# Kernel tuning notes

Hardware: AMD Instinct MI355X
Metric: run time of the kernel (lower is better)

The kernel has to match this reference:

```python
import jax, jax.numpy as jnp
import numpy as np

B, D = 8192, 64   # batch, state_dim (even -> canonical symplectic L)
H = 2 * D         # entropy MLP hidden


def setup_inputs() -> dict:
    key = jax.random.key(0)
    ks = jax.random.split(key, 6)
    sD = 1.0 / np.sqrt(D)
    sH = 1.0 / np.sqrt(H)
    z  = jax.random.normal(ks[0], (B, D), dtype=jnp.float32)
    # entropy MLP: Linear(D, 2D) -> SiLU -> Linear(2D, 1)  (torch default init ~ U(-1/sqrt(fan_in), ..))
    W1 = jax.random.uniform(ks[1], (H, D), jnp.float32, -sD, sD)
    b1 = jax.random.uniform(ks[2], (H,),   jnp.float32, -sD, sD)
    W2 = jax.random.uniform(ks[3], (1, H), jnp.float32, -sH, sH)
    b2 = jax.random.uniform(ks[4], (1,),   jnp.float32, -sH, sH)
    # friction A = Linear(D, D, bias=False)
    Wf = jax.random.uniform(ks[5], (D, D), jnp.float32, -sD, sD)
    return {"z": z, "W1": W1, "b1": b1, "W2": W2, "b2": b2, "Wf": Wf}


def _generic_forward(z, W1, b1, W2, b2, Wf):
    # grad_E: E = 0.5*||z||^2  ->  grad_E = z
    grad_E = z

    # grad_S via autodiff through the learnable entropy MLP (matches torch.autograd.grad)
    def entropy_sum(zz):
        h = jax.nn.silu(zz @ W1.T + b1)      # (B, 2D)
        return ((h @ W2.T) + b2).sum()       # scalar
    grad_S = jax.grad(entropy_sum)(z)        # (B, D)

    # Reversible term: canonical symplectic L (state_dim even). L is exactly skew,
    # so the 0.5*(L - L^T) projection is a no-op. L @ grad_E = [grad_E_p, -grad_E_q].
    n = D // 2
    reversible = jnp.concatenate([grad_E[:, n:], -grad_E[:, :n]], axis=-1)  # (B, D)

    # Friction: A = z Wf^T ; M = diag(A)^T diag(A) = diag(A^2); symmetrize (no-op),
    # then PSD projection via eigh + eigenvalue clamp (faithful to _make_psd).
    a = z @ Wf.T                                    # (B, D)
    M = (a * a)[:, :, None] * jnp.eye(D, dtype=z.dtype)  # diag_embed, (B, D, D)
    w, V = jnp.linalg.eigh(M)                       # batched small eigh
    w = jnp.clip(w, 0.0, None)
    M_psd = jnp.einsum('bij,bj,bkj->bik', V, w, V)  # V diag(w) V^T

    irreversible = jnp.einsum('bij,bj->bi', M_psd, grad_S)  # (B, D)

    lambda_rev = 1.0
    lambda_irr = 1.0
    return lambda_rev * reversible + lambda_irr * irreversible


def reference(z, W1, b1, W2, b2, Wf):
    return _generic_forward(z, W1, b1, W2, b2, Wf)
```

## Files before the change

kernel.cpp:

```cpp
#include <hip/hip_runtime.h>
#include <hip/hip_bf16.h>

typedef __bf16 bf16x8 __attribute__((ext_vector_type(8)));
typedef float  f32x4  __attribute__((ext_vector_type(4)));

#define MFMA16(a,b,c) __builtin_amdgcn_mfma_f32_16x16x32_bf16((a),(b),(c),0,0,0)

constexpr int Bn = 8192, Dd = 64, Hh = 128, MT = 32;

__device__ __forceinline__ unsigned short f2bf(float f) {
    unsigned int u = __builtin_bit_cast(unsigned int, f);
    u = (u + 0x7FFFu + ((u >> 16) & 1u)) >> 16;
    return (unsigned short)u;
}

__device__ __forceinline__ bf16x8 ld8(const unsigned short* p) {
    return *(const bf16x8*)p;
}

__global__ __launch_bounds__(256) void gnl_kernel(
    const float* __restrict__ z, const float* __restrict__ W1,
    const float* __restrict__ b1, const float* __restrict__ W2,
    const float* __restrict__ Wf, float* __restrict__ out)
{
    __shared__ unsigned short sh[29184];
    __shared__ float b1f[128];
    __shared__ float w2f[128];
    unsigned short* W1b = sh;
    unsigned short* Wfb = sh + 9216;
    unsigned short* Zb  = sh + 13824;
    unsigned short* W1T = sh + 16128;
    unsigned short* Gb  = sh + 24832;

    const int tid  = threadIdx.x;
    const int row0 = blockIdx.x * MT;

    {
        const float4* gv = (const float4*)W1;
        for (int i = tid; i < (Hh * Dd) / 4; i += 256) {
            float4 v = gv[i];
            int e = i << 2, j = e >> 6, d = e & 63;
            unsigned short c0 = f2bf(v.x), c1 = f2bf(v.y), c2 = f2bf(v.z), c3 = f2bf(v.w);
            *(ushort4*)(W1b + j * 72 + d) = make_ushort4(c0, c1, c2, c3);
            W1T[(d + 0) * 136 + j] = c0;
            W1T[(d + 1) * 136 + j] = c1;
            W1T[(d + 2) * 136 + j] = c2;
            W1T[(d + 3) * 136 + j] = c3;
        }
        gv = (const float4*)Wf;
        for (int i = tid; i < (Dd * Dd) / 4; i += 256) {
            float4 v = gv[i];
            int e = i << 2, j = e >> 6, d = e & 63;
            *(ushort4*)(Wfb + j * 72 + d) =
                make_ushort4(f2bf(v.x), f2bf(v.y), f2bf(v.z), f2bf(v.w));
        }
        gv = (const float4*)(z + (size_t)row0 * Dd);
        for (int i = tid; i < (MT * Dd) / 4; i += 256) {
            float4 v = gv[i];
            int e = i << 2, r = e >> 6, d = e & 63;
            *(ushort4*)(Zb + r * 72 + d) =
                make_ushort4(f2bf(v.x), f2bf(v.y), f2bf(v.z), f2bf(v.w));
        }
        if (tid < 128) { b1f[tid] = b1[tid]; w2f[tid] = W2[tid]; }
    }
    __syncthreads();

    const int lane = tid & 63, w = tid >> 6;
    const int l15 = lane & 15, q = lane >> 4;
    const int mt = w & 1;

    const int zoff = (mt * 16 + l15) * 72 + q * 8;
    bf16x8 za0 = ld8(Zb + zoff);
    bf16x8 za1 = ld8(Zb + zoff + 32);

    {
        const int ntb = (w >> 1) * 4;
        for (int nt = 0; nt < 4; ++nt) {
            const int jc = (ntb + nt) * 16 + l15;
            const unsigned short* wp = W1b + jc * 72 + q * 8;
            f32x4 acc = {0.f, 0.f, 0.f, 0.f};
            acc = MFMA16(za0, ld8(wp), acc);
            acc = MFMA16(za1, ld8(wp + 32), acc);
            const float bj = b1f[jc], w2j = w2f[jc];
            #pragma unroll
            for (int r = 0; r < 4; ++r) {
                float u = acc[r] + bj;
                float s = 1.f / (1.f + __expf(-u));
                float g = w2j * (s * (1.f + u * (1.f - s)));
                Gb[(mt * 16 + q * 4 + r) * 136 + jc] = f2bf(g);
            }
        }
    }
    __syncthreads();

    {
        const int goff = (mt * 16 + l15) * 136 + q * 8;
        bf16x8 ga0 = ld8(Gb + goff);
        bf16x8 ga1 = ld8(Gb + goff + 32);
        bf16x8 ga2 = ld8(Gb + goff + 64);
        bf16x8 ga3 = ld8(Gb + goff + 96);
        const int ntb = (w >> 1) * 2;
        for (int nt = 0; nt < 2; ++nt) {
            const int dc = (ntb + nt) * 16 + l15;
            const unsigned short* wt = W1T + dc * 136 + q * 8;
            f32x4 gs = {0.f, 0.f, 0.f, 0.f};
            gs = MFMA16(ga0, ld8(wt), gs);
            gs = MFMA16(ga1, ld8(wt + 32), gs);
            gs = MFMA16(ga2, ld8(wt + 64), gs);
            gs = MFMA16(ga3, ld8(wt + 96), gs);
            const unsigned short* wfp = Wfb + dc * 72 + q * 8;
            f32x4 av = {0.f, 0.f, 0.f, 0.f};
            av = MFMA16(za0, ld8(wfp), av);
            av = MFMA16(za1, ld8(wfp + 32), av);
            const bool  lo  = dc < 32;
            const int   src = lo ? dc + 32 : dc - 32;
            const float sgn = lo ? 1.f : -1.f;
            #pragma unroll
            for (int r = 0; r < 4; ++r) {
                const int rr = row0 + mt * 16 + q * 4 + r;
                float rev = sgn * z[(size_t)rr * Dd + src];
                float a = av[r];
                out[(size_t)rr * Dd + dc] = rev + a * a * gs[r];
            }
        }
    }
}

extern "C" void kernel_launch(void* const* d_in, const int* in_sizes, int n_in,
                              void* d_out, int out_size, void* d_ws, size_t ws_size,
                              hipStream_t stream)
{
    const float* z  = (const float*)d_in[0];
    const float* W1 = (const float*)d_in[1];
    const float* b1 = (const float*)d_in[2];
    const float* W2 = (const float*)d_in[3];
    const float* Wf = (const float*)d_in[5];
    float* out = (float*)d_out;
    gnl_kernel<<<Bn / MT, 256, 0, stream>>>(z, W1, b1, W2, Wf, out);
}
```

Baseline: 68.96 us.

## Precompute bf16 weight image once and DMA it into LDS per block

A separate prep kernel converts W1, W1^T, Wf, b1 and W2 once into a padded bf16 image in workspace. The main kernel then copies that image straight into LDS with global_load_lds instead of having every block convert and transpose the weights itself. The row tile is halved to 16 so each block does less work and more blocks run. The cost is a second kernel launch, a dependency between the two kernels, and every block still re-reading about 45KB of weights.

```diff
diff --git a/kernel.cpp b/kernel.cpp
--- a/kernel.cpp
+++ b/kernel.cpp
@@ -6,7 +6,11 @@
 
 #define MFMA16(a,b,c) __builtin_amdgcn_mfma_f32_16x16x32_bf16((a),(b),(c),0,0,0)
 
-constexpr int Bn = 8192, Dd = 64, Hh = 128, MT = 32;
+constexpr int Bn = 8192, Dd = 64, MT = 16;
+
+constexpr int OFF_WFB = 18432, OFF_W1T = 27648, OFF_B1 = 45056;
+constexpr int IMG_BYTES  = 46080;
+constexpr int IMG_CHUNKS = IMG_BYTES / 1024;
 
 __device__ __forceinline__ unsigned short f2bf(float f) {
     unsigned int u = __builtin_bit_cast(unsigned int, f);
@@ -14,114 +18,121 @@
     return (unsigned short)u;
 }
 
-__device__ __forceinline__ bf16x8 ld8(const unsigned short* p) {
-    return *(const bf16x8*)p;
+__device__ __forceinline__ void gload_lds16(const void* g, void* l) {
+    __builtin_amdgcn_global_load_lds(
+        (const __attribute__((address_space(1))) unsigned int*)g,
+        (__attribute__((address_space(3))) unsigned int*)l, 16, 0, 0);
+}
+
+__global__ __launch_bounds__(256) void prep_kernel(
+    const float* __restrict__ W1, const float* __restrict__ b1,
+    const float* __restrict__ W2, const float* __restrict__ Wf,
+    unsigned short* __restrict__ ws)
+{
+    int i = blockIdx.x * 256 + threadIdx.x;
+    unsigned short* W1b = ws;
+    unsigned short* Wfb = ws + OFF_WFB / 2;
+    unsigned short* W1T = ws + OFF_W1T / 2;
+    float* bw = (float*)(ws + OFF_B1 / 2);
+    if (i < 2048) {
+        float4 v = ((const float4*)W1)[i];
+        int e = i << 2, j = e >> 6, d = e & 63;
+        unsigned short c0 = f2bf(v.x), c1 = f2bf(v.y), c2 = f2bf(v.z), c3 = f2bf(v.w);
+        *(ushort4*)(W1b + j * 72 + d) = make_ushort4(c0, c1, c2, c3);
+        W1T[(d + 0) * 136 + j] = c0;
+        W1T[(d + 1) * 136 + j] = c1;
+        W1T[(d + 2) * 136 + j] = c2;
+        W1T[(d + 3) * 136 + j] = c3;
+    } else if (i < 3072) {
+        int k = i - 2048;
+        float4 v = ((const float4*)Wf)[k];
+        int e = k << 2, j = e >> 6, d = e & 63;
+        *(ushort4*)(Wfb + j * 72 + d) =
+            make_ushort4(f2bf(v.x), f2bf(v.y), f2bf(v.z), f2bf(v.w));
+    } else if (i < 3200) {
+        bw[i - 3072] = b1[i - 3072];
+    } else if (i < 3328) {
+        bw[128 + i - 3200] = W2[i - 3200];
+    }
 }
 
 __global__ __launch_bounds__(256) void gnl_kernel(
-    const float* __restrict__ z, const float* __restrict__ W1,
-    const float* __restrict__ b1, const float* __restrict__ W2,
-    const float* __restrict__ Wf, float* __restrict__ out)
+    const float* __restrict__ z, const unsigned short* __restrict__ wsimg,
+    float* __restrict__ out)
 {
-    __shared__ unsigned short sh[29184];
-    __shared__ float b1f[128];
-    __shared__ float w2f[128];
+    __shared__ unsigned short sh[26368];
     unsigned short* W1b = sh;
     unsigned short* Wfb = sh + 9216;
-    unsigned short* Zb  = sh + 13824;
-    unsigned short* W1T = sh + 16128;
-    unsigned short* Gb  = sh + 24832;
+    unsigned short* W1T = sh + 13824;
+    const float* b1f = (const float*)(sh + 22528);
+    const float* w2f = (const float*)(sh + 22784);
+    unsigned short* Zb = sh + 23040;
+    unsigned short* Gb = sh + 24192;
 
     const int tid  = threadIdx.x;
+    const int lane = tid & 63, wv = tid >> 6;
+    const int l15 = lane & 15, q = lane >> 4;
     const int row0 = blockIdx.x * MT;
 
+    for (int c = wv; c < IMG_CHUNKS; c += 4) {
+        gload_lds16((const char*)wsimg + c * 1024 + lane * 16,
+                    (char*)sh + c * 1024);
+    }
     {
-        const float4* gv = (const float4*)W1;
-        for (int i = tid; i < (Hh * Dd) / 4; i += 256) {
-            float4 v = gv[i];
-            int e = i << 2, j = e >> 6, d = e & 63;
-            unsigned short c0 = f2bf(v.x), c1 = f2bf(v.y), c2 = f2bf(v.z), c3 = f2bf(v.w);
-            *(ushort4*)(W1b + j * 72 + d) = make_ushort4(c0, c1, c2, c3);
-            W1T[(d + 0) * 136 + j] = c0;
-            W1T[(d + 1) * 136 + j] = c1;
-            W1T[(d + 2) * 136 + j] = c2;
-            W1T[(d + 3) * 136 + j] = c3;
-        }
-        gv = (const float4*)Wf;
-        for (int i = tid; i < (Dd * Dd) / 4; i += 256) {
-            float4 v = gv[i];
-            int e = i << 2, j = e >> 6, d = e & 63;
-            *(ushort4*)(Wfb + j * 72 + d) =
-                make_ushort4(f2bf(v.x), f2bf(v.y), f2bf(v.z), f2bf(v.w));
-        }
-        gv = (const float4*)(z + (size_t)row0 * Dd);
-        for (int i = tid; i < (MT * Dd) / 4; i += 256) {
-            float4 v = gv[i];
-            int e = i << 2, r = e >> 6, d = e & 63;
-            *(ushort4*)(Zb + r * 72 + d) =
-                make_ushort4(f2bf(v.x), f2bf(v.y), f2bf(v.z), f2bf(v.w));
-        }
-        if (tid < 128) { b1f[tid] = b1[tid]; w2f[tid] = W2[tid]; }
+        float4 v = ((const float4*)(z + (size_t)row0 * Dd))[tid];
+        int e = tid << 2, r = e >> 6, d = e & 63;
+        *(ushort4*)(Zb + r * 72 + d) =
+            make_ushort4(f2bf(v.x), f2bf(v.y), f2bf(v.z), f2bf(v.w));
     }
     __syncthreads();
 
-    const int lane = tid & 63, w = tid >> 6;
-    const int l15 = lane & 15, q = lane >> 4;
-    const int mt = w & 1;
+    const int zoff = l15 * 72 + q * 8;
+    bf16x8 za0 = *(const bf16x8*)(Zb + zoff);
+    bf16x8 za1 = *(const bf16x8*)(Zb + zoff + 32);
 
-    const int zoff = (mt * 16 + l15) * 72 + q * 8;
-    bf16x8 za0 = ld8(Zb + zoff);
-    bf16x8 za1 = ld8(Zb + zoff + 32);
-
-    {
-        const int ntb = (w >> 1) * 4;
-        for (int nt = 0; nt < 4; ++nt) {
-            const int jc = (ntb + nt) * 16 + l15;
-            const unsigned short* wp = W1b + jc * 72 + q * 8;
-            f32x4 acc = {0.f, 0.f, 0.f, 0.f};
-            acc = MFMA16(za0, ld8(wp), acc);
-            acc = MFMA16(za1, ld8(wp + 32), acc);
-            const float bj = b1f[jc], w2j = w2f[jc];
-            #pragma unroll
-            for (int r = 0; r < 4; ++r) {
-                float u = acc[r] + bj;
-                float s = 1.f / (1.f + __expf(-u));
-                float g = w2j * (s * (1.f + u * (1.f - s)));
-                Gb[(mt * 16 + q * 4 + r) * 136 + jc] = f2bf(g);
-            }
+    for (int nt = 0; nt < 2; ++nt) {
+        const int jc = (wv * 2 + nt) * 16 + l15;
+        const unsigned short* wp = W1b + jc * 72 + q * 8;
+        f32x4 acc = {0.f, 0.f, 0.f, 0.f};
+        acc = MFMA16(za0, *(const bf16x8*)wp, acc);
+        acc = MFMA16(za1, *(const bf16x8*)(wp + 32), acc);
+        const float bj = b1f[jc], w2j = w2f[jc];
+        #pragma unroll
+        for (int r = 0; r < 4; ++r) {
+            float u = acc[r] + bj;
+            float s = 1.f / (1.f + __expf(-u));
+            float g = w2j * (s * (1.f + u * (1.f - s)));
+            Gb[(q * 4 + r) * 136 + jc] = f2bf(g);
         }
     }
     __syncthreads();
 
     {
-        const int goff = (mt * 16 + l15) * 136 + q * 8;
-        bf16x8 ga0 = ld8(Gb + goff);
-        bf16x8 ga1 = ld8(Gb + goff + 32);
-        bf16x8 ga2 = ld8(Gb + goff + 64);
-        bf16x8 ga3 = ld8(Gb + goff + 96);
-        const int ntb = (w >> 1) * 2;
-        for (int nt = 0; nt < 2; ++nt) {
-            const int dc = (ntb + nt) * 16 + l15;
-            const unsigned short* wt = W1T + dc * 136 + q * 8;
-            f32x4 gs = {0.f, 0.f, 0.f, 0.f};
-            gs = MFMA16(ga0, ld8(wt), gs);
-            gs = MFMA16(ga1, ld8(wt + 32), gs);
-            gs = MFMA16(ga2, ld8(wt + 64), gs);
-            gs = MFMA16(ga3, ld8(wt + 96), gs);
-            const unsigned short* wfp = Wfb + dc * 72 + q * 8;
-            f32x4 av = {0.f, 0.f, 0.f, 0.f};
-            av = MFMA16(za0, ld8(wfp), av);
-            av = MFMA16(za1, ld8(wfp + 32), av);
-            const bool  lo  = dc < 32;
-            const int   src = lo ? dc + 32 : dc - 32;
-            const float sgn = lo ? 1.f : -1.f;
-            #pragma unroll
-            for (int r = 0; r < 4; ++r) {
-                const int rr = row0 + mt * 16 + q * 4 + r;
-                float rev = sgn * z[(size_t)rr * Dd + src];
-                float a = av[r];
-                out[(size_t)rr * Dd + dc] = rev + a * a * gs[r];
-            }
+        const int goff = l15 * 136 + q * 8;
+        bf16x8 ga0 = *(const bf16x8*)(Gb + goff);
+        bf16x8 ga1 = *(const bf16x8*)(Gb + goff + 32);
+        bf16x8 ga2 = *(const bf16x8*)(Gb + goff + 64);
+        bf16x8 ga3 = *(const bf16x8*)(Gb + goff + 96);
+        const int dc = wv * 16 + l15;
+        const unsigned short* wt = W1T + dc * 136 + q * 8;
+        f32x4 gs = {0.f, 0.f, 0.f, 0.f};
+        gs = MFMA16(ga0, *(const bf16x8*)wt, gs);
+        gs = MFMA16(ga1, *(const bf16x8*)(wt + 32), gs);
+        gs = MFMA16(ga2, *(const bf16x8*)(wt + 64), gs);
+        gs = MFMA16(ga3, *(const bf16x8*)(wt + 96), gs);
+        const unsigned short* wfp = Wfb + dc * 72 + q * 8;
+        f32x4 av = {0.f, 0.f, 0.f, 0.f};
+        av = MFMA16(za0, *(const bf16x8*)wfp, av);
+        av = MFMA16(za1, *(const bf16x8*)(wfp + 32), av);
+        const bool  lo  = dc < 32;
+        const int   src = lo ? dc + 32 : dc - 32;
+        const float sgn = lo ? 1.f : -1.f;
+        #pragma unroll
+        for (int r = 0; r < 4; ++r) {
+            const int rr = row0 + q * 4 + r;
+            float rev = sgn * z[(size_t)rr * Dd + src];
+            float a = av[r];
+            out[(size_t)rr * Dd + dc] = rev + a * a * gs[r];
         }
     }
 }
@@ -136,5 +147,8 @@
     const float* W2 = (const float*)d_in[3];
     const float* Wf = (const float*)d_in[5];
     float* out = (float*)d_out;
-    gnl_kernel<<<Bn / MT, 256, 0, stream>>>(z, W1, b1, W2, Wf, out);
+    unsigned short* ws = (unsigned short*)d_ws;
+
+    prep_kernel<<<13, 256, 0, stream>>>(W1, b1, W2, Wf, ws);
+    gnl_kernel<<<Bn / MT, 256, 0, stream>>>(z, ws, out);
 }
```

Result: no change. 68.42 us (-0.8%).
